# Kernel tuning notes

Measured on AMD Instinct MI355X. Metric: run time of the kernel, lower is better.

Reference implementation:

```python
import jax, jax.numpy as jnp
import numpy as np
from jax import lax

NBINS = 10
PP = 8            # pixels_per_cell
CPB = 2           # cells_per_block
MAX_ANGLE = float(np.pi)
EPS = 1e-5


def setup_inputs() -> dict:
    key = jax.random.key(0)
    img = jax.random.uniform(key, (32, 1, 512, 512), dtype=jnp.float32)
    # fixed Sobel-like gradient filters, same as the torch buffer: (2,1,3,3) OIHW
    m = np.array([[1.0, 0.0, -1.0], [2.0, 0.0, -2.0], [1.0, 0.0, -1.0]], dtype=np.float32)
    weight = jnp.asarray(np.stack([m, m.T])[:, None, :, :])
    return {"img": img, "weight": weight}


def reference(img, weight):
    n, _, H, W = img.shape
    # gradient conv: padding=1, stride=1 keeps spatial size
    gxy = lax.conv_general_dilated(
        img, weight, window_strides=(1, 1), padding=[(1, 1), (1, 1)],
        dimension_numbers=("NCHW", "OIHW", "NCHW"))  # (n,2,H,W)
    mag = jnp.sqrt(jnp.sum(gxy * gxy, axis=1))          # (n,H,W)
    phase = jnp.arctan2(gxy[:, 0], gxy[:, 1])           # (n,H,W)
    pbin = phase / MAX_ANGLE * NBINS
    fl = jnp.floor(pbin).astype(jnp.int32) % NBINS
    ce = jnp.ceil(pbin).astype(jnp.int32) % NBINS
    # scatter_ sets mag at floor bin (out starts at zeros), scatter_add_ adds (1-mag) at ceil bin
    oh_fl = jax.nn.one_hot(fl, NBINS, dtype=img.dtype)  # (n,H,W,nbins)
    oh_ce = jax.nn.one_hot(ce, NBINS, dtype=img.dtype)
    out = oh_fl * mag[..., None] + oh_ce * (1.0 - mag)[..., None]
    out = jnp.moveaxis(out, -1, 1)                      # (n,nbins,H,W)
    # avg pool with kernel==stride==PP, no padding -> reshape mean
    hc, wc = H // PP, W // PP
    out = out.reshape(n, NBINS, hc, PP, wc, PP).mean(axis=(3, 5))  # (n,nbins,hc,wc)
    # block normalization (L2-Hys); note: norms reduce over batch dim too, as in the source
    nbr, nbc = hc - CPB + 1, wc - CPB + 1
    blocks = jnp.stack(
        [jnp.stack([out[:, :, i:i + nbr, j:j + nbc] for j in range(CPB)], axis=2)
         for i in range(CPB)], axis=2)                  # (n,nbins,CPB,CPB,nbr,nbc)
    s = jnp.sum(blocks * blocks, axis=(0, 1, 2, 3), keepdims=True)
    v = blocks / jnp.sqrt(s + EPS * EPS)
    v = jnp.minimum(v, 0.2)
    s2 = jnp.sum(v * v, axis=(0, 1, 2, 3), keepdims=True)
    v = v / jnp.sqrt(s2 + EPS * EPS)
    return v.reshape(n, -1)  # feature_vector=True
```

## Files before the change

kernel.cpp:

```cpp
#include <hip/hip_runtime.h>
#include <math.h>

#define NBINS 10
#define NB    32
#define HH    512
#define WW    512
#define HC    64
#define WC    64
#define NBR   63
#define NBC   63
#define EPS2F 1e-10f

__global__ __launch_bounds__(256) void k_cellhist(const float* __restrict__ img,
                                                  float* __restrict__ cell,
                                                  float* __restrict__ Q) {
    const int cy = blockIdx.x;
    const int n  = blockIdx.y;
    const int t  = threadIdx.x;

    __shared__ float lds[10][516];

    const float* im = img + (size_t)n * HH * WW;
    const int gy0 = cy * 8 - 1;
    for (int idx = t; idx < 10 * 514; idx += 256) {
        int r  = idx / 514;
        int c  = idx - r * 514;
        int gr = gy0 + r, gc = c - 1;
        float v = 0.0f;
        if ((unsigned)gr < HH && (unsigned)gc < WW) v = im[gr * WW + gc];
        lds[r][c] = v;
    }
    __syncthreads();

    const float pi32 = (float)M_PI;
    const float S1 = 0.30901699f, C1 = 0.95105652f;
    const float S2 = 0.58778525f, C2 = 0.80901699f;
    const float S3 = 0.80901699f, C3 = 0.58778525f;
    const float S4 = 0.95105652f, C4 = 0.30901699f;

    const int cc  = t >> 2;
    const int sub = t & 3;
    const int r0  = 1 + 2 * sub;

    float R[4][10];
#pragma unroll
    for (int r = 0; r < 4; ++r) {
        const float* rowp = &lds[r0 - 1 + r][cc * 8];
        float4 v0 = *(const float4*)(rowp);
        float4 v1 = *(const float4*)(rowp + 4);
        float2 v2 = *(const float2*)(rowp + 8);
        R[r][0] = v0.x; R[r][1] = v0.y; R[r][2] = v0.z; R[r][3] = v0.w;
        R[r][4] = v1.x; R[r][5] = v1.y; R[r][6] = v1.z; R[r][7] = v1.w;
        R[r][8] = v2.x; R[r][9] = v2.y;
    }

    float hist[NBINS];
#pragma unroll
    for (int b = 0; b < NBINS; ++b) hist[b] = 0.0f;

#pragma unroll
    for (int ry = 0; ry < 2; ++ry) {
#pragma unroll
        for (int k = 0; k < 8; ++k) {
            float a  = R[ry    ][k    ];
            float b  = R[ry    ][k + 1];
            float c  = R[ry    ][k + 2];
            float d  = R[ry + 1][k    ];
            float f  = R[ry + 1][k + 2];
            float g  = R[ry + 2][k    ];
            float h  = R[ry + 2][k + 1];
            float i2 = R[ry + 2][k + 2];
            float gA = a;
            gA = gA - c;
            gA = gA + 2.0f * d;
            gA = gA - 2.0f * f;
            gA = gA + g;
            gA = gA - i2;
            float gB = a;
            gB = gB + 2.0f * b;
            gB = gB + c;
            gB = gB - g;
            gB = gB - 2.0f * h;
            gB = gB - i2;

            float mag = __builtin_amdgcn_sqrtf(gA * gA + gB * gB);

            float y = fabsf(gA), x = fabsf(gB);
            float cr1 = fmaf(y, C1, -(x * S1));
            float cr2 = fmaf(y, C2, -(x * S2));
            float cr3 = fmaf(y, C3, -(x * S3));
            float cr4 = fmaf(y, C4, -(x * S4));
            int idx = (cr1 > 0.0f) + (cr2 > 0.0f) + (cr3 > 0.0f) + (cr4 > 0.0f);
            float minc = fminf(fminf(y, x),
                               fminf(fminf(fabsf(cr1), fabsf(cr2)),
                                     fminf(fabsf(cr3), fabsf(cr4))));
            int flm, cem;
            if (minc > 3.2e-5f * mag) {
                bool same = (gA >= 0.0f) == (gB >= 0.0f);
                flm = same ? idx : 9 - idx;
                cem = flm + 1; if (cem == NBINS) cem = 0;
            } else {
                float phase = (float)atan2((double)gA, (double)gB);
                float pb = phase / pi32;
                pb = pb * 10.0f;
                int fl = (int)floorf(pb);
                int ce = (int)ceilf(pb);
                flm = fl % NBINS; if (flm < 0) flm += NBINS;
                cem = ce % NBINS; if (cem < 0) cem += NBINS;
            }
            hist[flm] += mag;
            hist[cem] += 1.0f - mag;
        }
    }

#pragma unroll
    for (int b = 0; b < NBINS; ++b) {
        hist[b] += __shfl_xor(hist[b], 1);
        hist[b] += __shfl_xor(hist[b], 2);
    }

#pragma unroll
    for (int bb = 0; bb < NBINS; ++bb) {
        if ((bb & 3) == sub)
            cell[(((size_t)n * NBINS + bb) * HC + cy) * WC + cc] = hist[bb] * 0.015625f;
    }
    if (sub == 0) {
        float q = 0.0f;
#pragma unroll
        for (int bb = 0; bb < NBINS; ++bb) {
            float cv = hist[bb] * 0.015625f;
            q = fmaf(cv, cv, q);
        }
        atomicAdd(&Q[cy * WC + cc], q);
    }
}

__global__ __launch_bounds__(256) void k_s2(const float* __restrict__ cell,
                                            const float* __restrict__ Q,
                                            float* __restrict__ s2) {
    const int i     = blockIdx.x;
    const int chunk = blockIdx.y;
    const int t     = threadIdx.x;
    const int j     = t & 63;
    const int sub   = t >> 6;
    if (j >= NBC) return;
    float s = Q[i * WC + j] + Q[i * WC + j + 1] +
              Q[(i + 1) * WC + j] + Q[(i + 1) * WC + j + 1];
    float w = 1.0f / sqrtf(s + EPS2F);
    float acc = 0.0f;
    const int nb0 = (chunk * 4 + sub) * 10;
    for (int nb = nb0; nb < nb0 + 10; ++nb) {
        const float* base = cell + ((size_t)nb * HC + i) * WC + j;
        float v00 = base[0], v01 = base[1];
        float v10 = base[WC], v11 = base[WC + 1];
        v00 = fminf(v00 * w, 0.2f); acc = fmaf(v00, v00, acc);
        v01 = fminf(v01 * w, 0.2f); acc = fmaf(v01, v01, acc);
        v10 = fminf(v10 * w, 0.2f); acc = fmaf(v10, v10, acc);
        v11 = fminf(v11 * w, 0.2f); acc = fmaf(v11, v11, acc);
    }
    atomicAdd(&s2[i * NBC + j], acc);
}

__global__ void k_inv(const float* __restrict__ Q, const float* __restrict__ s2,
                      float* __restrict__ inv1, float* __restrict__ inv2) {
    int idx = blockIdx.x * blockDim.x + threadIdx.x;
    if (idx >= NBR * NBC) return;
    int i = idx / NBC, j = idx - i * NBC;
    float s = Q[i * WC + j] + Q[i * WC + j + 1] +
              Q[(i + 1) * WC + j] + Q[(i + 1) * WC + j + 1];
    inv1[idx] = 1.0f / sqrtf(s + EPS2F);
    inv2[idx] = 1.0f / sqrtf(s2[idx] + EPS2F);
}

__global__ void k_out(const float* __restrict__ cell,
                      const float* __restrict__ inv1,
                      const float* __restrict__ inv2,
                      float* __restrict__ out) {
    int idx = blockIdx.x * blockDim.x + threadIdx.x;
    const int total = NB * NBINS * 2 * 2 * NBR * NBC;
    if (idx >= total) return;
    int ij  = idx % (NBR * NBC);
    int tmp = idx / (NBR * NBC);
    int j   = ij % NBC;
    int i   = ij / NBC;
    int dj  = tmp % 2;   tmp /= 2;
    int di  = tmp % 2;   tmp /= 2;
    int b   = tmp % NBINS;
    int n   = tmp / NBINS;
    float v = cell[(((size_t)n * NBINS + b) * HC + i + di) * WC + j + dj] * inv1[ij];
    v = fminf(v, 0.2f);
    out[idx] = v * inv2[ij];
}

extern "C" void kernel_launch(void* const* d_in, const int* in_sizes, int n_in,
                              void* d_out, int out_size, void* d_ws, size_t ws_size,
                              hipStream_t stream) {
    const float* img = (const float*)d_in[0];
    float* out = (float*)d_out;

    float* cell = (float*)d_ws;
    float* Q    = cell + (size_t)NB * NBINS * HC * WC;
    float* s2   = Q + HC * WC;
    float* inv1 = s2 + NBR * NBC;
    float* inv2 = inv1 + NBR * NBC;

    hipMemsetAsync(Q, 0, (size_t)(HC * WC + NBR * NBC) * sizeof(float), stream);
    hipLaunchKernelGGL(k_cellhist, dim3(HC, NB), dim3(256), 0, stream, img, cell, Q);
    hipLaunchKernelGGL(k_s2, dim3(NBR, 8), dim3(256), 0, stream, cell, Q, s2);
    hipLaunchKernelGGL(k_inv, dim3(16), dim3(256), 0, stream, Q, s2, inv1, inv2);
    const int total = NB * NBINS * 2 * 2 * NBR * NBC;
    hipLaunchKernelGGL(k_out, dim3((total + 255) / 256), dim3(256), 0, stream,
                       cell, inv1, inv2, out);
}
```

Measured before the change: 130.1 us.

## Replace atomic norm accumulation with single fused per-row normalization kernel

Drops the atomicAdd of per-cell squared sums from the histogram kernel, along with the memset and the separate s2 and inv kernels. A new k_norm kernel gets one block per block-row; it reduces both the first L2 norm and the clipped second norm in shared memory and writes inv1 and inv2 directly. This removes atomics and two launches, but k_norm runs only 63 blocks and reads the cell array twice. The histogram kernel also gets a min-blocks hint of 4 in its launch bounds.

```diff
diff --git a/kernel.cpp b/kernel.cpp
--- a/kernel.cpp
+++ b/kernel.cpp
@@ -11,9 +11,8 @@
 #define NBC   63
 #define EPS2F 1e-10f
 
-__global__ __launch_bounds__(256) void k_cellhist(const float* __restrict__ img,
-                                                  float* __restrict__ cell,
-                                                  float* __restrict__ Q) {
+__global__ __launch_bounds__(256, 4) void k_cellhist(const float* __restrict__ img,
+                                                     float* __restrict__ cell) {
     const int cy = blockIdx.x;
     const int n  = blockIdx.y;
     const int t  = threadIdx.x;
@@ -124,52 +123,56 @@
         if ((bb & 3) == sub)
             cell[(((size_t)n * NBINS + bb) * HC + cy) * WC + cc] = hist[bb] * 0.015625f;
     }
+}
+
+__global__ __launch_bounds__(256) void k_norm(const float* __restrict__ cell,
+                                              float* __restrict__ inv1,
+                                              float* __restrict__ inv2) {
+    const int i   = blockIdx.x;
+    const int t   = threadIdx.x;
+    const int j   = t & 63;
+    const int sub = t >> 6;
+    const int j1  = (j < 63) ? 1 : 0;
+
+    __shared__ float red[4][64];
+    __shared__ float wsh[64];
+
+    float acc = 0.0f;
+    for (int s0 = sub; s0 < NB * NBINS; s0 += 4) {
+        const float* base = cell + ((size_t)s0 * HC + i) * WC + j;
+        float v00 = base[0],  v01 = base[j1];
+        float v10 = base[WC], v11 = base[WC + j1];
+        acc = fmaf(v00, v00, acc);
+        acc = fmaf(v01, v01, acc);
+        acc = fmaf(v10, v10, acc);
+        acc = fmaf(v11, v11, acc);
+    }
+    red[sub][j] = acc;
+    __syncthreads();
     if (sub == 0) {
-        float q = 0.0f;
-#pragma unroll
-        for (int bb = 0; bb < NBINS; ++bb) {
-            float cv = hist[bb] * 0.015625f;
-            q = fmaf(cv, cv, q);
-        }
-        atomicAdd(&Q[cy * WC + cc], q);
-    }
-}
-
-__global__ __launch_bounds__(256) void k_s2(const float* __restrict__ cell,
-                                            const float* __restrict__ Q,
-                                            float* __restrict__ s2) {
-    const int i     = blockIdx.x;
-    const int chunk = blockIdx.y;
-    const int t     = threadIdx.x;
-    const int j     = t & 63;
-    const int sub   = t >> 6;
-    if (j >= NBC) return;
-    float s = Q[i * WC + j] + Q[i * WC + j + 1] +
-              Q[(i + 1) * WC + j] + Q[(i + 1) * WC + j + 1];
-    float w = 1.0f / sqrtf(s + EPS2F);
-    float acc = 0.0f;
-    const int nb0 = (chunk * 4 + sub) * 10;
-    for (int nb = nb0; nb < nb0 + 10; ++nb) {
-        const float* base = cell + ((size_t)nb * HC + i) * WC + j;
-        float v00 = base[0], v01 = base[1];
-        float v10 = base[WC], v11 = base[WC + 1];
-        v00 = fminf(v00 * w, 0.2f); acc = fmaf(v00, v00, acc);
-        v01 = fminf(v01 * w, 0.2f); acc = fmaf(v01, v01, acc);
-        v10 = fminf(v10 * w, 0.2f); acc = fmaf(v10, v10, acc);
-        v11 = fminf(v11 * w, 0.2f); acc = fmaf(v11, v11, acc);
-    }
-    atomicAdd(&s2[i * NBC + j], acc);
-}
-
-__global__ void k_inv(const float* __restrict__ Q, const float* __restrict__ s2,
-                      float* __restrict__ inv1, float* __restrict__ inv2) {
-    int idx = blockIdx.x * blockDim.x + threadIdx.x;
-    if (idx >= NBR * NBC) return;
-    int i = idx / NBC, j = idx - i * NBC;
-    float s = Q[i * WC + j] + Q[i * WC + j + 1] +
-              Q[(i + 1) * WC + j] + Q[(i + 1) * WC + j + 1];
-    inv1[idx] = 1.0f / sqrtf(s + EPS2F);
-    inv2[idx] = 1.0f / sqrtf(s2[idx] + EPS2F);
+        float s = red[0][j] + red[1][j] + red[2][j] + red[3][j];
+        wsh[j] = 1.0f / sqrtf(s + EPS2F);
+    }
+    __syncthreads();
+    const float w = wsh[j];
+
+    float acc2 = 0.0f;
+    for (int s0 = sub; s0 < NB * NBINS; s0 += 4) {
+        const float* base = cell + ((size_t)s0 * HC + i) * WC + j;
+        float v00 = base[0],  v01 = base[j1];
+        float v10 = base[WC], v11 = base[WC + j1];
+        v00 = fminf(v00 * w, 0.2f); acc2 = fmaf(v00, v00, acc2);
+        v01 = fminf(v01 * w, 0.2f); acc2 = fmaf(v01, v01, acc2);
+        v10 = fminf(v10 * w, 0.2f); acc2 = fmaf(v10, v10, acc2);
+        v11 = fminf(v11 * w, 0.2f); acc2 = fmaf(v11, v11, acc2);
+    }
+    red[sub][j] = acc2;
+    __syncthreads();
+    if (sub == 0 && j < NBC) {
+        float s2 = red[0][j] + red[1][j] + red[2][j] + red[3][j];
+        inv1[i * NBC + j] = w;
+        inv2[i * NBC + j] = 1.0f / sqrtf(s2 + EPS2F);
+    }
 }
 
 __global__ void k_out(const float* __restrict__ cell,
@@ -199,15 +202,11 @@
     float* out = (float*)d_out;
 
     float* cell = (float*)d_ws;
-    float* Q    = cell + (size_t)NB * NBINS * HC * WC;
-    float* s2   = Q + HC * WC;
-    float* inv1 = s2 + NBR * NBC;
+    float* inv1 = cell + (size_t)NB * NBINS * HC * WC;
     float* inv2 = inv1 + NBR * NBC;
 
-    hipMemsetAsync(Q, 0, (size_t)(HC * WC + NBR * NBC) * sizeof(float), stream);
-    hipLaunchKernelGGL(k_cellhist, dim3(HC, NB), dim3(256), 0, stream, img, cell, Q);
-    hipLaunchKernelGGL(k_s2, dim3(NBR, 8), dim3(256), 0, stream, cell, Q, s2);
-    hipLaunchKernelGGL(k_inv, dim3(16), dim3(256), 0, stream, Q, s2, inv1, inv2);
+    hipLaunchKernelGGL(k_cellhist, dim3(HC, NB), dim3(256), 0, stream, img, cell);
+    hipLaunchKernelGGL(k_norm, dim3(NBR), dim3(256), 0, stream, cell, inv1, inv2);
     const int total = NB * NBINS * 2 * 2 * NBR * NBC;
     hipLaunchKernelGGL(k_out, dim3((total + 255) / 256), dim3(256), 0, stream,
                        cell, inv1, inv2, out);
```

Result: slower. 153.6 us (+18.1%).

## Move Q reduction out of histogram kernel and cut atomic contention

Applied to the files above, without the earlier changes.

Removes the per-cell atomicAdd of squared cell values from the histogram kernel and computes Q in a separate kernel that reduces over batch and bins. Partial sums are combined in shared memory before a single atomic per block column. k_s2 gets twice as many blocks with shorter loops and the same shared-memory pre-reduction. Adds launch_bounds occupancy hint to the histogram kernel. This trades heavy same-address atomic contention (32 batches hitting each Q entry) for an extra kernel launch and a re-read of the cell buffer.

```diff
diff --git a/kernel.cpp b/kernel.cpp
--- a/kernel.cpp
+++ b/kernel.cpp
@@ -11,9 +11,8 @@
 #define NBC   63
 #define EPS2F 1e-10f
 
-__global__ __launch_bounds__(256) void k_cellhist(const float* __restrict__ img,
-                                                  float* __restrict__ cell,
-                                                  float* __restrict__ Q) {
+__global__ __launch_bounds__(256, 4) void k_cellhist(const float* __restrict__ img,
+                                                     float* __restrict__ cell) {
     const int cy = blockIdx.x;
     const int n  = blockIdx.y;
     const int t  = threadIdx.x;
@@ -124,15 +123,26 @@
         if ((bb & 3) == sub)
             cell[(((size_t)n * NBINS + bb) * HC + cy) * WC + cc] = hist[bb] * 0.015625f;
     }
-    if (sub == 0) {
-        float q = 0.0f;
-#pragma unroll
-        for (int bb = 0; bb < NBINS; ++bb) {
-            float cv = hist[bb] * 0.015625f;
-            q = fmaf(cv, cv, q);
-        }
-        atomicAdd(&Q[cy * WC + cc], q);
-    }
+}
+
+__global__ __launch_bounds__(256) void k_Q(const float* __restrict__ cell,
+                                           float* __restrict__ Q) {
+    const int i     = blockIdx.x;
+    const int chunk = blockIdx.y;
+    const int t     = threadIdx.x;
+    const int j     = t & 63;
+    const int sub   = t >> 6;
+    float acc = 0.0f;
+    const int s0 = (chunk * 4 + sub) * 20;
+    for (int s = s0; s < s0 + 20; ++s) {
+        float v = cell[((size_t)s * HC + i) * WC + j];
+        acc = fmaf(v, v, acc);
+    }
+    __shared__ float red[4][64];
+    red[sub][j] = acc;
+    __syncthreads();
+    if (sub == 0)
+        atomicAdd(&Q[i * WC + j], red[0][j] + red[1][j] + red[2][j] + red[3][j]);
 }
 
 __global__ __launch_bounds__(256) void k_s2(const float* __restrict__ cell,
@@ -143,22 +153,28 @@
     const int t     = threadIdx.x;
     const int j     = t & 63;
     const int sub   = t >> 6;
-    if (j >= NBC) return;
-    float s = Q[i * WC + j] + Q[i * WC + j + 1] +
-              Q[(i + 1) * WC + j] + Q[(i + 1) * WC + j + 1];
+    const int jj    = (j < NBC) ? j : (NBC - 1);
+
+    float s = Q[i * WC + jj] + Q[i * WC + jj + 1] +
+              Q[(i + 1) * WC + jj] + Q[(i + 1) * WC + jj + 1];
     float w = 1.0f / sqrtf(s + EPS2F);
+
     float acc = 0.0f;
-    const int nb0 = (chunk * 4 + sub) * 10;
-    for (int nb = nb0; nb < nb0 + 10; ++nb) {
-        const float* base = cell + ((size_t)nb * HC + i) * WC + j;
-        float v00 = base[0], v01 = base[1];
+    const int nb0 = (chunk * 4 + sub) * 5;
+    for (int nb = nb0; nb < nb0 + 5; ++nb) {
+        const float* base = cell + ((size_t)nb * HC + i) * WC + jj;
+        float v00 = base[0],  v01 = base[1];
         float v10 = base[WC], v11 = base[WC + 1];
         v00 = fminf(v00 * w, 0.2f); acc = fmaf(v00, v00, acc);
         v01 = fminf(v01 * w, 0.2f); acc = fmaf(v01, v01, acc);
         v10 = fminf(v10 * w, 0.2f); acc = fmaf(v10, v10, acc);
         v11 = fminf(v11 * w, 0.2f); acc = fmaf(v11, v11, acc);
     }
-    atomicAdd(&s2[i * NBC + j], acc);
+    __shared__ float red[4][64];
+    red[sub][j] = acc;
+    __syncthreads();
+    if (sub == 0 && j < NBC)
+        atomicAdd(&s2[i * NBC + j], red[0][j] + red[1][j] + red[2][j] + red[3][j]);
 }
 
 __global__ void k_inv(const float* __restrict__ Q, const float* __restrict__ s2,
@@ -205,8 +221,9 @@
     float* inv2 = inv1 + NBR * NBC;
 
     hipMemsetAsync(Q, 0, (size_t)(HC * WC + NBR * NBC) * sizeof(float), stream);
-    hipLaunchKernelGGL(k_cellhist, dim3(HC, NB), dim3(256), 0, stream, img, cell, Q);
-    hipLaunchKernelGGL(k_s2, dim3(NBR, 8), dim3(256), 0, stream, cell, Q, s2);
+    hipLaunchKernelGGL(k_cellhist, dim3(HC, NB), dim3(256), 0, stream, img, cell);
+    hipLaunchKernelGGL(k_Q, dim3(HC, 4), dim3(256), 0, stream, cell, Q);
+    hipLaunchKernelGGL(k_s2, dim3(NBR, 16), dim3(256), 0, stream, cell, Q, s2);
     hipLaunchKernelGGL(k_inv, dim3(16), dim3(256), 0, stream, Q, s2, inv1, inv2);
     const int total = NB * NBINS * 2 * 2 * NBR * NBC;
     hipLaunchKernelGGL(k_out, dim3((total + 255) / 256), dim3(256), 0, stream,
```

New measurement: 134.8 us. 3.6% more time.
